# Performance work log

Measured on AMD Instinct MI355X. Metric: run time of the kernel, lower is better.

The kernel has to match this reference:

```python
import jax, jax.numpy as jnp
import numpy as np

N_HEADS = 2
EPS = 1e-5
NEG_SLOPE = 0.02
N_CENTROIDS = 1024
RADII = (0.1, 0.2)
KS = (32, 64)


def fps(x, m):
    # Farthest point sampling (deterministic start at index 0). x: [B, C, N]
    B, C, N = x.shape
    def body(carry, _):
        distance, farthest = carry
        centroid = jnp.take_along_axis(x, jnp.broadcast_to(farthest[:, None, None], (B, C, 1)), axis=2)
        dist = jnp.sum((x - centroid) ** 2, axis=1)  # [B, N]
        distance = jnp.minimum(distance, dist)
        nxt = jnp.argmax(distance, axis=1).astype(jnp.int32)
        return (distance, nxt), farthest
    init = (jnp.full((B, N), 1e10, x.dtype), jnp.zeros((B,), jnp.int32))
    _, idxs = jax.lax.scan(body, init, None, length=m)
    return idxs.T  # [B, m]


def ball_group(x, centroids, radius, k):
    # x: [B, C, N], centroids: [B, C, M] -> (idx [B,M,k] int32, mask [B,M,k] bool)
    B, C, N = x.shape
    M = centroids.shape[2]
    d = (jnp.sum(x * x, axis=1)[:, None, :]
         - 2.0 * jnp.einsum('bcm,bcn->bmn', centroids, x)
         + jnp.sum(centroids * centroids, axis=1)[:, :, None])  # [B, M, N]
    idx = jnp.broadcast_to(jnp.arange(N, dtype=jnp.int32)[None, None, :], (B, M, N))
    idx = jnp.where(d > radius * radius, N, idx)
    idx = -jax.lax.top_k(-idx, k)[0]  # k smallest indices, ascending (matches torch.topk largest=False)
    mask = idx == N
    first = jnp.where(idx[:, :, :1] == N, 0, idx[:, :, :1])
    idx = jnp.where(mask, jnp.broadcast_to(first, idx.shape), idx)
    return idx, mask


def attention_mix(x, y, mask, wq, wk, wv, wo):
    # x: [B, C, K] centroids, y: [B, C, K, Np] groups, mask: [B, K, Np]
    B, C, K = x.shape
    Np = y.shape[3]
    H = N_HEADS
    q = jnp.einsum('oc,bck->bok', wq, x).reshape(B, H, C, K)
    kk = jnp.einsum('oc,bckn->bokn', wk, y).reshape(B, H, C, K, Np)
    v = jnp.einsum('oc,bckn->bokn', wv, y).reshape(B, H, C, K, Np)
    w = jnp.einsum('bhck,bhckn->bhkn', q, kk) / (C ** 0.5)
    w = jnp.where(mask[:, None, :, :], -1e9, w)
    w = jax.nn.softmax(w, axis=3)
    o = jnp.einsum('bhkn,bhckn->bhck', w, v).reshape(B, H * C, K)
    return jnp.einsum('oc,bck->bok', wo, o) + x


def conv_bn(x, w, b, g, beta, act):
    # 1x1 Conv1d + BatchNorm1d (training-mode batch stats) + optional LeakyReLU(0.02)
    x = jnp.einsum('oc,bck->bok', w, x) + b[None, :, None]
    mu = jnp.mean(x, axis=(0, 2), keepdims=True)
    var = jnp.var(x, axis=(0, 2), keepdims=True)
    x = (x - mu) * jax.lax.rsqrt(var + EPS) * g[None, :, None] + beta[None, :, None]
    return jnp.where(x > 0, x, NEG_SLOPE * x) if act else x


def pointnet_msg(xyz, point_features, attn_params, mlp_params):
    support = jnp.concatenate([xyz, point_features], axis=1)  # [B, 32, N]
    B, Cs, N = support.shape
    M = N_CENTROIDS
    cidx = fps(support, M)  # [B, M]
    centroids = jnp.take_along_axis(support, jnp.broadcast_to(cidx[:, None, :], (B, Cs, M)), axis=2)
    new_xyz = jnp.take_along_axis(xyz, jnp.broadcast_to(cidx[:, None, :], (B, 3, M)), axis=2)
    feats = []
    for s, (radius, k) in enumerate(zip(RADII, KS)):
        idx, mask = ball_group(support, centroids, radius, k)  # [B, M, k]
        gidx = jnp.broadcast_to(idx.reshape(B, 1, M * k), (B, Cs, M * k))
        group = jnp.take_along_axis(support, gidx, axis=2).reshape(B, Cs, M, k)
        group = group - centroids[:, :, :, None]
        f = attention_mix(centroids, group, mask, *attn_params[s])
        (w0, b0, g0, t0), (w1, b1, g1, t1) = mlp_params[s]
        f = conv_bn(f, w0, b0, g0, t0, act=True)
        f = conv_bn(f, w1, b1, g1, t1, act=False)
        feats.append(f)
    return new_xyz, jnp.concatenate(feats, axis=1)  # [B,3,M], [B,256,M]


def setup_inputs() -> dict:
    key = jax.random.key(0)
    ks = jax.random.split(key, 32)
    B, N, C = 4, 16384, 32
    d = {}
    d['xyz'] = jax.random.uniform(ks[0], (B, 3, N), jnp.float32)
    d['point_features'] = jax.random.normal(ks[1], (B, C - 3, N), jnp.float32)
    i = 2
    for s in range(2):
        d[f'aq{s}'] = 0.05 * jax.random.normal(ks[i], (64, 32), jnp.float32); i += 1
        d[f'ak{s}'] = 0.05 * jax.random.normal(ks[i], (64, 32), jnp.float32); i += 1
        d[f'av{s}'] = 0.05 * jax.random.normal(ks[i], (64, 32), jnp.float32); i += 1
        d[f'ao{s}'] = 0.05 * jax.random.normal(ks[i], (32, 64), jnp.float32); i += 1
        d[f'mw{s}0'] = 0.05 * jax.random.normal(ks[i], (64, 32), jnp.float32); i += 1
        d[f'mb{s}0'] = jnp.zeros((64,), jnp.float32)
        d[f'mg{s}0'] = jnp.ones((64,), jnp.float32)
        d[f'mbt{s}0'] = jnp.zeros((64,), jnp.float32)
        d[f'mw{s}1'] = 0.05 * jax.random.normal(ks[i], (128, 64), jnp.float32); i += 1
        d[f'mb{s}1'] = jnp.zeros((128,), jnp.float32)
        d[f'mg{s}1'] = jnp.ones((128,), jnp.float32)
        d[f'mbt{s}1'] = jnp.zeros((128,), jnp.float32)
    return d


def reference(xyz, point_features,
              aq0, ak0, av0, ao0, mw00, mb00, mg00, mbt00, mw01, mb01, mg01, mbt01,
              aq1, ak1, av1, ao1, mw10, mb10, mg10, mbt10, mw11, mb11, mg11, mbt11):
    attn_params = (((aq0, ak0, av0, ao0)), ((aq1, ak1, av1, ao1)))
    mlp_params = (((mw00, mb00, mg00, mbt00), (mw01, mb01, mg01, mbt01)),
                  ((mw10, mb10, mg10, mbt10), (mw11, mb11, mg11, mbt11)))
    return pointnet_msg(xyz, point_features, attn_params, mlp_params)
```

## Files before the change

### kernel.cpp

```cpp
#include <hip/hip_runtime.h>
#include <hip/hip_bf16.h>


static constexpr int Bb = 4;
static constexpr int Npts = 16384;
static constexpr int Mc = 1024;
static constexpr int NBLK = 16;
static constexpr int OUT_EXPECT = 12288 + 1048576;
#define BN_EPS 1e-5f
#define SLOPE 0.02f
#define SCOPE_AGT __HIP_MEMORY_SCOPE_AGENT

static constexpr size_t OFF_STATS = 33024;
static constexpr size_t OFF_NORM  = 36864;
static constexpr size_t ZERO_BYTES = 65536;
static constexpr size_t OFF_CIDX  = 65536;
static constexpr size_t OFF_IDX0  = 81920;
static constexpr size_t OFF_CNT0  = 344064;
static constexpr size_t OFF_IDX1  = 360448;
static constexpr size_t OFF_CNT1  = 884736;
static constexpr size_t OFF_ATTN  = 901120;
static constexpr size_t OFF_Z0    = 1163264;
static constexpr size_t WS_REQUIRED = 1687552;
static constexpr size_t OFF_FSLOT = 901120;
static constexpr size_t FSLOT_BYTES = (size_t)Bb * Mc * NBLK * 8;

__device__ __forceinline__ float sup_at(const float* xyz, const float* pf,
                                        int b, int c, int n) {
  return (c < 3) ? xyz[((size_t)b*3 + c)*Npts + n]
                 : pf[((size_t)b*29 + (c-3))*Npts + n];
}

__device__ __forceinline__ float sanf(float v, float repl) {
  if (!(v == v) || fabsf(v) > 1e30f) v = repl;
  return v;
}

__global__ __launch_bounds__(256) void fill_kernel(float* out, int n, float val) {
  int i = blockIdx.x * 256 + threadIdx.x;
  if (i < n) out[i] = val;
}

__global__ __launch_bounds__(512, 2) void fps_kernel(
    const float* __restrict__ xyz, const float* __restrict__ pf,
    int* __restrict__ cidx, unsigned long long* __restrict__ slots) {
  const int blk = blockIdx.x;
  const int b = blk >> 4;
  const int sb = blk & (NBLK - 1);
  const int tid = threadIdx.x;
  const int lane = tid & 63, wid = tid >> 6;
  float f0[32], f1[32];
  const int p0 = sb * 1024 + tid;
  const int p1 = p0 + 512;
  float d0 = 1e10f, d1 = 1e10f;
#pragma unroll
  for (int c = 0; c < 32; ++c) {
    f0[c] = sup_at(xyz, pf, b, c, p0);
    f1[c] = sup_at(xyz, pf, b, c, p1);
  }
  __shared__ float cf[32];
  __shared__ unsigned long long red[8];
  if (sb == 0 && tid == 0) cidx[b * Mc] = 0;
  if (tid < 32) cf[tid] = sup_at(xyz, pf, b, tid, 0);
  __syncthreads();
  unsigned long long* slotb = slots + (size_t)b * Mc * NBLK;
  for (int it = 0; it < Mc - 1; ++it) {
    float cc[32];
#pragma unroll
    for (int c = 0; c < 32; ++c) cc[c] = cf[c];
    {
      float d = 0.f, e = 0.f;
#pragma unroll
      for (int c = 0; c < 32; ++c) {
        float t0 = f0[c] - cc[c];
        float s0 = __fmul_rn(t0, t0);
        d = (c == 0) ? s0 : __fadd_rn(d, s0);
        float t1 = f1[c] - cc[c];
        float s1 = __fmul_rn(t1, t1);
        e = (c == 0) ? s1 : __fadd_rn(e, s1);
      }
      d0 = fminf(d0, d);
      d1 = fminf(d1, e);
    }
    float bd; int bp;
    if (d0 >= d1) { bd = d0; bp = p0; } else { bd = d1; bp = p1; }
    unsigned long long v =
        ((unsigned long long)__float_as_uint(bd) << 32) | (unsigned int)(~(unsigned int)bp);
#pragma unroll
    for (int d = 32; d; d >>= 1) {
      unsigned long long o = __shfl_xor(v, d, 64);
      if (o > v) v = o;
    }
    if (lane == 0) red[wid] = v;
    __syncthreads();
    if (tid == 0) {
      unsigned long long vb = red[0];
#pragma unroll
      for (int w = 1; w < 8; ++w) if (red[w] > vb) vb = red[w];
      atomicMax(&slotb[(size_t)it * NBLK + sb], vb);
    }
    if (wid == 0) {
      unsigned long long myv = 0;
      if (lane < NBLK) {
        const unsigned long long* sp = &slotb[(size_t)it * NBLK + lane];
        while ((myv = __hip_atomic_load(sp, __ATOMIC_RELAXED, SCOPE_AGT)) == 0ull)
          __builtin_amdgcn_s_sleep(1);
      }
      unsigned long long mv = myv;
#pragma unroll
      for (int d = 8; d; d >>= 1) {
        unsigned long long o = __shfl_xor(mv, d, 16);
        if (o > mv) mv = o;
      }
      unsigned long long vwin = __shfl(mv, 0, 64);
      int idxWin = (int)(~(unsigned int)(vwin & 0xffffffffu)) & (Npts - 1);
      if (lane < 32) cf[lane] = sup_at(xyz, pf, b, lane, idxWin);
      if (lane == 0 && sb == 0) cidx[b * Mc + it + 1] = idxWin;
    }
    __syncthreads();
  }
}

__global__ __launch_bounds__(256) void gather_kernel(
    const float* __restrict__ xyz, const int* __restrict__ cidx,
    float* __restrict__ oxyz, int out_size) {
  int idx = blockIdx.x * 256 + threadIdx.x;
  if (idx >= out_size || idx >= 12288) return;
  int m = idx & (Mc - 1);
  int t = idx >> 10;
  int b = t / 3;
  int ci = cidx[b * Mc + m] & (Npts - 1);
  oxyz[idx] = sanf(xyz[(size_t)t * Npts + ci], 888.0f);
}

__global__ __launch_bounds__(256) void ball_kernel(
    const float* __restrict__ xyz, const float* __restrict__ pf,
    const int* __restrict__ cidx,
    unsigned short* __restrict__ idx0, int* __restrict__ cnt0,
    unsigned short* __restrict__ idx1, int* __restrict__ cnt1) {
  const int b = blockIdx.x >> 6;
  const int mt = blockIdx.x & 63;
  const int tid = threadIdx.x;
  __shared__ float cf[16][32];
  __shared__ float csq[16];
  __shared__ unsigned int ent[16][128];
  __shared__ int lcnt[16];
  for (int i = tid; i < 16 * 32; i += 256) {
    int ml = i >> 5, c = i & 31;
    int ci = cidx[b * Mc + mt * 16 + ml] & (Npts - 1);
    cf[ml][c] = sup_at(xyz, pf, b, c, ci);
  }
  if (tid < 16) lcnt[tid] = 0;
  __syncthreads();
  if (tid < 16) {
    float a = 0.f;
#pragma unroll
    for (int c = 0; c < 32; ++c) a = fmaf(cf[tid][c], cf[tid][c], a);
    csq[tid] = a;
  }
  __syncthreads();
  for (int ch = 0; ch < Npts / 256; ++ch) {
    int p = ch * 256 + tid;
    float x[32];
#pragma unroll
    for (int c = 0; c < 32; ++c) x[c] = sup_at(xyz, pf, b, c, p);
    float sp = 0.f;
#pragma unroll
    for (int c = 0; c < 32; ++c) sp = fmaf(x[c], x[c], sp);
#pragma unroll 4
    for (int ml = 0; ml < 16; ++ml) {
      float dot = 0.f;
#pragma unroll
      for (int c = 0; c < 32; ++c) dot = fmaf(cf[ml][c], x[c], dot);
      float d = sp - 2.0f * dot + csq[ml];
      if (d <= 0.04f) {
        int pos = atomicAdd(&lcnt[ml], 1);
        if (pos < 128) ent[ml][pos] = (unsigned int)p | (d <= 0.01f ? 0x80000000u : 0u);
      }
    }
  }
  __syncthreads();
  if (tid < 16) {
    int ml = tid;
    int nn = lcnt[ml]; if (nn > 128) nn = 128;
    for (int i = 1; i < nn; ++i) {
      unsigned int e = ent[ml][i]; unsigned int key = e & 0x7fffffffu;
      int j = i - 1;
      while (j >= 0 && (ent[ml][j] & 0x7fffffffu) > key) { ent[ml][j+1] = ent[ml][j]; --j; }
      ent[ml][j+1] = e;
    }
    int gm = b * Mc + mt * 16 + ml;
    int c1 = nn < 64 ? nn : 64;
    unsigned short first1 = nn > 0 ? (unsigned short)(ent[ml][0] & 0x7fffffffu) : 0;
    unsigned short* o1 = idx1 + (size_t)gm * 64;
    for (int j = 0; j < 64; ++j)
      o1[j] = j < c1 ? (unsigned short)(ent[ml][j] & 0x7fffffffu) : first1;
    cnt1[gm] = c1;
    unsigned short* o0 = idx0 + (size_t)gm * 32;
    int c0 = 0; unsigned short first0 = 0;
    for (int i = 0; i < nn && c0 < 32; ++i) {
      if (ent[ml][i] & 0x80000000u) {
        unsigned short nv = (unsigned short)(ent[ml][i] & 0x7fffffffu);
        if (c0 == 0) first0 = nv;
        o0[c0++] = nv;
      }
    }
    for (int j = c0; j < 32; ++j) o0[j] = first0;
    cnt0[gm] = c0;
  }
}

template <int K>
__global__ __launch_bounds__(256) void attn_kernel(
    const float* __restrict__ xyz, const float* __restrict__ pf,
    const int* __restrict__ cidx,
    const unsigned short* __restrict__ idxS, const int* __restrict__ cntS,
    const float* __restrict__ wq, const float* __restrict__ wk,
    const float* __restrict__ wv, const float* __restrict__ wo,
    __hip_bfloat16* __restrict__ outA) {
  __shared__ float WqL[64*33], WkL[64*33], WvL[64*33], WoL[32*65];
  __shared__ float xv[4][32];
  __shared__ float qv[4][64];
  __shared__ float yb[4][2][32];
  __shared__ float ov[4][64];
  __shared__ int cns[4];
  const int tid = threadIdx.x;
  const int wid = tid >> 6, lane = tid & 63;
  const int gid = blockIdx.x;
  const int b = gid >> 8;
  const int m = ((gid & 255) << 2) + wid;
  for (int i = tid; i < 2048; i += 256) {
    int r = i >> 5, c = i & 31;
    WqL[r*33 + c] = wq[i];
    WkL[r*33 + c] = wk[i];
    WvL[r*33 + c] = wv[i];
    int ro = i >> 6, co = i & 63;
    WoL[ro*65 + co] = wo[i];
  }
  if (lane < 32) {
    int ci = cidx[b * Mc + m] & (Npts - 1);
    xv[wid][lane] = sup_at(xyz, pf, b, lane, ci);
  }
  if (lane == 0) cns[wid] = cntS[b * Mc + m];
  __syncthreads();
  {
    float acc = 0.f;
#pragma unroll
    for (int c = 0; c < 32; ++c) acc = fmaf(WqL[lane*33 + c], xv[wid][c], acc);
    qv[wid][lane] = acc;
  }
  __syncthreads();
  int cnt = cns[wid];
  cnt = cnt < 1 ? 1 : (cnt > K ? K : cnt);
  const int jj = lane < K ? lane : 0;
  int nj = (int)idxS[((size_t)b*Mc + m)*K + jj] & (Npts - 1);
  float y[32];
#pragma unroll
  for (int c = 0; c < 32; ++c)
    y[c] = sup_at(xyz, pf, b, c, nj) - xv[wid][c];
  float w0 = 0.f, w1 = 0.f;
#pragma unroll 2
  for (int r = 0; r < 32; ++r) {
    float k0 = 0.f, k1 = 0.f;
#pragma unroll
    for (int c = 0; c < 32; ++c) {
      k0 = fmaf(WkL[r*33 + c], y[c], k0);
      k1 = fmaf(WkL[(r+32)*33 + c], y[c], k1);
    }
    w0 = fmaf(qv[wid][r], k0, w0);
    w1 = fmaf(qv[wid][r+32], k1, w1);
  }
  const float iscale = 0.17677669529663689f;
  w0 *= iscale; w1 *= iscale;
  if (lane >= cnt) { w0 = -1e9f; w1 = -1e9f; }
  float mx0 = w0, mx1 = w1;
#pragma unroll
  for (int d = K/2; d; d >>= 1) {
    mx0 = fmaxf(mx0, __shfl_xor(mx0, d, K));
    mx1 = fmaxf(mx1, __shfl_xor(mx1, d, K));
  }
  float e0 = __expf(w0 - mx0), e1 = __expf(w1 - mx1);
  float s0 = e0, s1 = e1;
#pragma unroll
  for (int d = K/2; d; d >>= 1) {
    s0 += __shfl_xor(s0, d, K);
    s1 += __shfl_xor(s1, d, K);
  }
  float wn0 = e0 / s0, wn1 = e1 / s1;
#pragma unroll
  for (int c = 0; c < 32; ++c) {
    float t0 = wn0 * y[c], t1 = wn1 * y[c];
#pragma unroll
    for (int d = K/2; d; d >>= 1) {
      t0 += __shfl_xor(t0, d, K);
      t1 += __shfl_xor(t1, d, K);
    }
    if (lane == 0) { yb[wid][0][c] = t0; yb[wid][1][c] = t1; }
  }
  __syncthreads();
  {
    const int h = lane >> 5;
    float a2 = 0.f;
#pragma unroll
    for (int c = 0; c < 32; ++c) a2 = fmaf(WvL[lane*33 + c], yb[wid][h][c], a2);
    ov[wid][lane] = a2;
  }
  __syncthreads();
  if (lane < 32) {
    float a3 = 0.f;
#pragma unroll
    for (int r = 0; r < 64; ++r) a3 = fmaf(WoL[lane*65 + r], ov[wid][r], a3);
    outA[((size_t)b*32 + lane)*Mc + m] = __float2bfloat16(a3 + xv[wid][lane]);
  }
}

__global__ __launch_bounds__(256) void conv0_kernel(
    const __hip_bfloat16* __restrict__ inA, const float* __restrict__ w0,
    const float* __restrict__ b0, __hip_bfloat16* __restrict__ z0,
    float* __restrict__ ssum, float* __restrict__ ssq) {
  int idx = blockIdx.x * 256 + threadIdx.x;
  int m = idx & (Mc - 1);
  int r = (idx >> 10) & 63;
  int b = idx >> 16;
  float acc = b0[r];
#pragma unroll
  for (int c = 0; c < 32; ++c)
    acc = fmaf(w0[r*32 + c], __bfloat162float(inA[((size_t)b*32 + c)*Mc + m]), acc);
  z0[((size_t)b*64 + r)*Mc + m] = __float2bfloat16(acc);
  float s = acc, q = acc * acc;
#pragma unroll
  for (int d = 32; d; d >>= 1) { s += __shfl_down(s, d, 64); q += __shfl_down(q, d, 64); }
  if ((threadIdx.x & 63) == 0) { atomicAdd(&ssum[r], s); atomicAdd(&ssq[r], q); }
}

__global__ void bnfin_kernel(const float* __restrict__ ssum, const float* __restrict__ ssq,
    const float* __restrict__ g, const float* __restrict__ beta,
    float* __restrict__ A, float* __restrict__ Bn, int nch, float invn) {
  int r = threadIdx.x;
  if (r < nch) {
    float mu = ssum[r] * invn;
    float var = ssq[r] * invn - mu * mu;
    if (var < 0.f) var = 0.f;
    float a = g[r] * rsqrtf(var + BN_EPS);
    A[r] = a;
    Bn[r] = beta[r] - mu * a;
  }
}

template <bool WRITE>
__global__ __launch_bounds__(256) void conv1_kernel(
    const __hip_bfloat16* __restrict__ z0, const float* __restrict__ A0, const float* __restrict__ B0n,
    const float* __restrict__ w1, const float* __restrict__ b1,
    float* __restrict__ ssum, float* __restrict__ ssq,
    const float* __restrict__ A1, const float* __restrict__ B1n,
    float* __restrict__ outAll, int chOff, int out_size) {
  int idx = blockIdx.x * 256 + threadIdx.x;
  int m = idx & (Mc - 1);
  int r2 = (idx >> 10) & 127;
  int b = idx >> 17;
  float acc = b1[r2];
#pragma unroll 8
  for (int r = 0; r < 64; ++r) {
    float u = fmaf(__bfloat162float(z0[((size_t)b*64 + r)*Mc + m]), A0[r], B0n[r]);
    u = u > 0.f ? u : SLOPE * u;
    acc = fmaf(w1[r2*64 + r], u, acc);
  }
  if (WRITE) {
    float v = fmaf(acc, A1[r2], B1n[r2]);
    size_t oidx = 12288 + ((size_t)b*256 + chOff + r2)*Mc + m;
    if (oidx < (size_t)out_size) outAll[oidx] = sanf(v, 777.0f);
  } else {
    float s = acc, q = acc * acc;
#pragma unroll
    for (int d = 32; d; d >>= 1) { s += __shfl_down(s, d, 64); q += __shfl_down(q, d, 64); }
    if ((threadIdx.x & 63) == 0) { atomicAdd(&ssum[r2], s); atomicAdd(&ssq[r2], q); }
  }
}

extern "C" void kernel_launch(void* const* d_in, const int* in_sizes, int n_in,
                              void* d_out, int out_size, void* d_ws, size_t ws_size,
                              hipStream_t stream) {
  float* outb = (float*)d_out;
  int fillBlocks = (out_size + 255) / 256;
  if (n_in != 26 || in_sizes[0] != Bb*3*Npts || in_sizes[1] != Bb*29*Npts
      || in_sizes[2] != 2048) {
    fill_kernel<<<fillBlocks, 256, 0, stream>>>(outb, out_size, 7777.0f);
    return;
  }
  if (out_size != OUT_EXPECT) {
    fill_kernel<<<fillBlocks, 256, 0, stream>>>(outb, out_size, 23456.0f);
    return;
  }
  if (ws_size < WS_REQUIRED) {
    fill_kernel<<<fillBlocks, 256, 0, stream>>>(outb, out_size, 12345.0f);
    return;
  }
  const float* xyz = (const float*)d_in[0];
  const float* pf  = (const float*)d_in[1];
  char* ws = (char*)d_ws;
  int* cidx = (int*)(ws + OFF_CIDX);
  unsigned short* idx0 = (unsigned short*)(ws + OFF_IDX0);
  int* cnt0 = (int*)(ws + OFF_CNT0);
  unsigned short* idx1 = (unsigned short*)(ws + OFF_IDX1);
  int* cnt1 = (int*)(ws + OFF_CNT1);
  unsigned long long* fslots = (unsigned long long*)(ws + OFF_FSLOT);
  __hip_bfloat16* attn = (__hip_bfloat16*)(ws + OFF_ATTN);
  __hip_bfloat16* z0 = (__hip_bfloat16*)(ws + OFF_Z0);

  hipMemsetAsync(ws, 0, ZERO_BYTES, stream);
  hipMemsetAsync(ws + OFF_FSLOT, 0, FSLOT_BYTES, stream);
  fps_kernel<<<Bb*NBLK, 512, 0, stream>>>(xyz, pf, cidx, fslots);
  ball_kernel<<<Bb*64, 256, 0, stream>>>(xyz, pf, cidx, idx0, cnt0, idx1, cnt1);

  for (int s = 0; s < 2; ++s) {
    const float* aq = (const float*)d_in[2 + s*12 + 0];
    const float* ak = (const float*)d_in[2 + s*12 + 1];
    const float* av = (const float*)d_in[2 + s*12 + 2];
    const float* ao = (const float*)d_in[2 + s*12 + 3];
    const float* w0 = (const float*)d_in[2 + s*12 + 4];
    const float* b0 = (const float*)d_in[2 + s*12 + 5];
    const float* g0 = (const float*)d_in[2 + s*12 + 6];
    const float* t0 = (const float*)d_in[2 + s*12 + 7];
    const float* w1 = (const float*)d_in[2 + s*12 + 8];
    const float* b1 = (const float*)d_in[2 + s*12 + 9];
    const float* g1 = (const float*)d_in[2 + s*12 + 10];
    const float* t1 = (const float*)d_in[2 + s*12 + 11];
    float* st = (float*)(ws + OFF_STATS) + (size_t)s*384;
    float* nrm = (float*)(ws + OFF_NORM) + (size_t)s*384;
    float *sum0 = st, *sq0 = st + 64, *sum1 = st + 128, *sq1 = st + 256;
    float *A0 = nrm, *B0n = nrm + 64, *A1 = nrm + 128, *B1n = nrm + 256;
    if (s == 0)
      attn_kernel<32><<<Bb*Mc/4, 256, 0, stream>>>(xyz, pf, cidx, idx0, cnt0, aq, ak, av, ao, attn);
    else
      attn_kernel<64><<<Bb*Mc/4, 256, 0, stream>>>(xyz, pf, cidx, idx1, cnt1, aq, ak, av, ao, attn);
    conv0_kernel<<<Bb*64*Mc/256, 256, 0, stream>>>(attn, w0, b0, z0, sum0, sq0);
    bnfin_kernel<<<1, 64, 0, stream>>>(sum0, sq0, g0, t0, A0, B0n, 64, 1.0f/4096.0f);
    conv1_kernel<false><<<Bb*128*Mc/256, 256, 0, stream>>>(z0, A0, B0n, w1, b1, sum1, sq1,
                                                           nullptr, nullptr, nullptr, 0, out_size);
    bnfin_kernel<<<1, 128, 0, stream>>>(sum1, sq1, g1, t1, A1, B1n, 128, 1.0f/4096.0f);
    conv1_kernel<true><<<Bb*128*Mc/256, 256, 0, stream>>>(z0, A0, B0n, w1, b1, nullptr, nullptr,
                                                          A1, B1n, outb, s*128, out_size);
  }
  gather_kernel<<<48, 256, 0, stream>>>(xyz, cidx, outb, out_size);
}
```

Before: 2.758 ms.

## Prefetch candidate centroids in parallel in FPS and fuse BN finalize into conv1

In the FPS loop, every block's threads now each poll one of the 16 per-block slots and gather that candidate's 32 features into shared memory. The winner is then chosen from shared memory, which removes a serial dependent global load after the cross-block reduction on the critical path of each of the 1023 iterations. Separately, the BN finalize kernels are folded into the conv1 kernels. When the workspace is large enough, the pre-BN conv1 output is cached in a new z1 buffer so the write pass skips recomputation. This costs extra polling traffic, shared memory and z1 storage, and z1 is only used when the workspace exceeds the previously required size.

```diff
diff --git a/kernel.cpp b/kernel.cpp
--- a/kernel.cpp
+++ b/kernel.cpp
@@ -12,7 +12,6 @@
 #define SCOPE_AGT __HIP_MEMORY_SCOPE_AGENT
 
 static constexpr size_t OFF_STATS = 33024;
-static constexpr size_t OFF_NORM  = 36864;
 static constexpr size_t ZERO_BYTES = 65536;
 static constexpr size_t OFF_CIDX  = 65536;
 static constexpr size_t OFF_IDX0  = 81920;
@@ -24,6 +23,8 @@
 static constexpr size_t WS_REQUIRED = 1687552;
 static constexpr size_t OFF_FSLOT = 901120;
 static constexpr size_t FSLOT_BYTES = (size_t)Bb * Mc * NBLK * 8;
+static constexpr size_t OFF_Z1 = 1687552;
+static constexpr size_t WS_Z1_REQUIRED = OFF_Z1 + (size_t)Bb * 128 * Mc * 4;
 
 __device__ __forceinline__ float sup_at(const float* xyz, const float* pf,
                                         int b, int c, int n) {
@@ -59,7 +60,9 @@
     f1[c] = sup_at(xyz, pf, b, c, p1);
   }
   __shared__ float cf[32];
+  __shared__ float cand[NBLK][32];
   __shared__ unsigned long long red[8];
+  __shared__ unsigned long long cval[NBLK];
   if (sb == 0 && tid == 0) cidx[b * Mc] = 0;
   if (tid < 32) cf[tid] = sup_at(xyz, pf, b, tid, 0);
   __syncthreads();
@@ -99,24 +102,24 @@
       for (int w = 1; w < 8; ++w) if (red[w] > vb) vb = red[w];
       atomicMax(&slotb[(size_t)it * NBLK + sb], vb);
     }
-    if (wid == 0) {
-      unsigned long long myv = 0;
-      if (lane < NBLK) {
-        const unsigned long long* sp = &slotb[(size_t)it * NBLK + lane];
-        while ((myv = __hip_atomic_load(sp, __ATOMIC_RELAXED, SCOPE_AGT)) == 0ull)
-          __builtin_amdgcn_s_sleep(1);
-      }
-      unsigned long long mv = myv;
-#pragma unroll
-      for (int d = 8; d; d >>= 1) {
-        unsigned long long o = __shfl_xor(mv, d, 16);
-        if (o > mv) mv = o;
-      }
-      unsigned long long vwin = __shfl(mv, 0, 64);
-      int idxWin = (int)(~(unsigned int)(vwin & 0xffffffffu)) & (Npts - 1);
-      if (lane < 32) cf[lane] = sup_at(xyz, pf, b, lane, idxWin);
-      if (lane == 0 && sb == 0) cidx[b * Mc + it + 1] = idxWin;
-    }
+    {
+      const int myslot = (wid << 1) | (lane >> 5);
+      const unsigned long long* sp = &slotb[(size_t)it * NBLK + myslot];
+      unsigned long long myv;
+      while ((myv = __hip_atomic_load(sp, __ATOMIC_RELAXED, SCOPE_AGT)) == 0ull)
+        __builtin_amdgcn_s_sleep(1);
+      int pc = (int)(~(unsigned int)(myv & 0xffffffffu)) & (Npts - 1);
+      cand[myslot][lane & 31] = sup_at(xyz, pf, b, lane & 31, pc);
+      if ((lane & 31) == 0) cval[myslot] = myv;
+    }
+    __syncthreads();
+    unsigned long long vwin = cval[0]; int wblk = 0;
+#pragma unroll
+    for (int w = 1; w < NBLK; ++w)
+      if (cval[w] > vwin) { vwin = cval[w]; wblk = w; }
+    if (tid < 32) cf[tid] = cand[wblk][tid];
+    if (sb == 0 && tid == 0)
+      cidx[b * Mc + it + 1] = (int)(~(unsigned int)(vwin & 0xffffffffu)) & (Npts - 1);
     __syncthreads();
   }
 }
@@ -333,48 +336,89 @@
   if ((threadIdx.x & 63) == 0) { atomicAdd(&ssum[r], s); atomicAdd(&ssq[r], q); }
 }
 
-__global__ void bnfin_kernel(const float* __restrict__ ssum, const float* __restrict__ ssq,
-    const float* __restrict__ g, const float* __restrict__ beta,
-    float* __restrict__ A, float* __restrict__ Bn, int nch, float invn) {
-  int r = threadIdx.x;
-  if (r < nch) {
-    float mu = ssum[r] * invn;
-    float var = ssq[r] * invn - mu * mu;
+__global__ __launch_bounds__(256) void conv1_stats_kernel(
+    const __hip_bfloat16* __restrict__ z0,
+    const float* __restrict__ ssum0, const float* __restrict__ ssq0,
+    const float* __restrict__ g0, const float* __restrict__ t0,
+    const float* __restrict__ w1, const float* __restrict__ b1,
+    float* __restrict__ z1,
+    float* __restrict__ ssum1, float* __restrict__ ssq1) {
+  __shared__ float A0s[64], B0s[64];
+  int tid = threadIdx.x;
+  if (tid < 64) {
+    float mu = ssum0[tid] * (1.0f/4096.0f);
+    float var = ssq0[tid] * (1.0f/4096.0f) - mu * mu;
     if (var < 0.f) var = 0.f;
-    float a = g[r] * rsqrtf(var + BN_EPS);
-    A[r] = a;
-    Bn[r] = beta[r] - mu * a;
-  }
-}
-
-template <bool WRITE>
-__global__ __launch_bounds__(256) void conv1_kernel(
-    const __hip_bfloat16* __restrict__ z0, const float* __restrict__ A0, const float* __restrict__ B0n,
-    const float* __restrict__ w1, const float* __restrict__ b1,
-    float* __restrict__ ssum, float* __restrict__ ssq,
-    const float* __restrict__ A1, const float* __restrict__ B1n,
-    float* __restrict__ outAll, int chOff, int out_size) {
-  int idx = blockIdx.x * 256 + threadIdx.x;
+    float a = g0[tid] * rsqrtf(var + BN_EPS);
+    A0s[tid] = a;
+    B0s[tid] = t0[tid] - mu * a;
+  }
+  __syncthreads();
+  int idx = blockIdx.x * 256 + tid;
   int m = idx & (Mc - 1);
   int r2 = (idx >> 10) & 127;
   int b = idx >> 17;
   float acc = b1[r2];
 #pragma unroll 8
   for (int r = 0; r < 64; ++r) {
-    float u = fmaf(__bfloat162float(z0[((size_t)b*64 + r)*Mc + m]), A0[r], B0n[r]);
+    float u = fmaf(__bfloat162float(z0[((size_t)b*64 + r)*Mc + m]), A0s[r], B0s[r]);
     u = u > 0.f ? u : SLOPE * u;
     acc = fmaf(w1[r2*64 + r], u, acc);
   }
-  if (WRITE) {
-    float v = fmaf(acc, A1[r2], B1n[r2]);
-    size_t oidx = 12288 + ((size_t)b*256 + chOff + r2)*Mc + m;
-    if (oidx < (size_t)out_size) outAll[oidx] = sanf(v, 777.0f);
+  if (z1) z1[idx] = acc;
+  float s = acc, q = acc * acc;
+#pragma unroll
+  for (int d = 32; d; d >>= 1) { s += __shfl_down(s, d, 64); q += __shfl_down(q, d, 64); }
+  if ((tid & 63) == 0) { atomicAdd(&ssum1[r2], s); atomicAdd(&ssq1[r2], q); }
+}
+
+__global__ __launch_bounds__(256) void conv1_write_kernel(
+    const __hip_bfloat16* __restrict__ z0, const float* __restrict__ z1,
+    const float* __restrict__ ssum0, const float* __restrict__ ssq0,
+    const float* __restrict__ g0, const float* __restrict__ t0,
+    const float* __restrict__ w1, const float* __restrict__ b1,
+    const float* __restrict__ ssum1, const float* __restrict__ ssq1,
+    const float* __restrict__ g1, const float* __restrict__ t1,
+    float* __restrict__ outAll, int chOff, int out_size) {
+  __shared__ float A0s[64], B0s[64];
+  __shared__ float ab1[2];
+  int tid = threadIdx.x;
+  int idx = blockIdx.x * 256 + tid;
+  int m = idx & (Mc - 1);
+  int r2 = (idx >> 10) & 127;
+  int b = idx >> 17;
+  if (!z1 && tid < 64) {
+    float mu = ssum0[tid] * (1.0f/4096.0f);
+    float var = ssq0[tid] * (1.0f/4096.0f) - mu * mu;
+    if (var < 0.f) var = 0.f;
+    float a = g0[tid] * rsqrtf(var + BN_EPS);
+    A0s[tid] = a;
+    B0s[tid] = t0[tid] - mu * a;
+  }
+  if (tid == 0) {
+    float mu = ssum1[r2] * (1.0f/4096.0f);
+    float var = ssq1[r2] * (1.0f/4096.0f) - mu * mu;
+    if (var < 0.f) var = 0.f;
+    float a = g1[r2] * rsqrtf(var + BN_EPS);
+    ab1[0] = a;
+    ab1[1] = t1[r2] - mu * a;
+  }
+  __syncthreads();
+  float acc;
+  if (z1) {
+    acc = z1[idx];
   } else {
-    float s = acc, q = acc * acc;
-#pragma unroll
-    for (int d = 32; d; d >>= 1) { s += __shfl_down(s, d, 64); q += __shfl_down(q, d, 64); }
-    if ((threadIdx.x & 63) == 0) { atomicAdd(&ssum[r2], s); atomicAdd(&ssq[r2], q); }
-  }
+    acc = b1[r2];
+#pragma unroll 8
+    for (int r = 0; r < 64; ++r) {
+      float u = fmaf(__bfloat162float(z0[((size_t)b*64 + r)*Mc + m]), A0s[r], B0s[r]);
+      u = u > 0.f ? u : SLOPE * u;
+      acc = fmaf(w1[r2*64 + r], u, acc);
+    }
+  }
+  float v = fmaf(acc, ab1[0], ab1[1]);
+  size_t oidx = 12288 + ((size_t)b*256 + chOff + r2)*Mc + m;
+  if (oidx < (size_t)out_size) outAll[oidx] = sanf(v, 777.0f);
 }
 
 extern "C" void kernel_launch(void* const* d_in, const int* in_sizes, int n_in,
@@ -406,6 +450,7 @@
   unsigned long long* fslots = (unsigned long long*)(ws + OFF_FSLOT);
   __hip_bfloat16* attn = (__hip_bfloat16*)(ws + OFF_ATTN);
   __hip_bfloat16* z0 = (__hip_bfloat16*)(ws + OFF_Z0);
+  float* z1 = (ws_size >= WS_Z1_REQUIRED) ? (float*)(ws + OFF_Z1) : nullptr;
 
   hipMemsetAsync(ws, 0, ZERO_BYTES, stream);
   hipMemsetAsync(ws + OFF_FSLOT, 0, FSLOT_BYTES, stream);
@@ -426,20 +471,17 @@
     const float* g1 = (const float*)d_in[2 + s*12 + 10];
     const float* t1 = (const float*)d_in[2 + s*12 + 11];
     float* st = (float*)(ws + OFF_STATS) + (size_t)s*384;
-    float* nrm = (float*)(ws + OFF_NORM) + (size_t)s*384;
     float *sum0 = st, *sq0 = st + 64, *sum1 = st + 128, *sq1 = st + 256;
-    float *A0 = nrm, *B0n = nrm + 64, *A1 = nrm + 128, *B1n = nrm + 256;
     if (s == 0)
       attn_kernel<32><<<Bb*Mc/4, 256, 0, stream>>>(xyz, pf, cidx, idx0, cnt0, aq, ak, av, ao, attn);
     else
       attn_kernel<64><<<Bb*Mc/4, 256, 0, stream>>>(xyz, pf, cidx, idx1, cnt1, aq, ak, av, ao, attn);
     conv0_kernel<<<Bb*64*Mc/256, 256, 0, stream>>>(attn, w0, b0, z0, sum0, sq0);
-    bnfin_kernel<<<1, 64, 0, stream>>>(sum0, sq0, g0, t0, A0, B0n, 64, 1.0f/4096.0f);
-    conv1_kernel<false><<<Bb*128*Mc/256, 256, 0, stream>>>(z0, A0, B0n, w1, b1, sum1, sq1,
-                                                           nullptr, nullptr, nullptr, 0, out_size);
-    bnfin_kernel<<<1, 128, 0, stream>>>(sum1, sq1, g1, t1, A1, B1n, 128, 1.0f/4096.0f);
-    conv1_kernel<true><<<Bb*128*Mc/256, 256, 0, stream>>>(z0, A0, B0n, w1, b1, nullptr, nullptr,
-                                                          A1, B1n, outb, s*128, out_size);
+    conv1_stats_kernel<<<Bb*128*Mc/256, 256, 0, stream>>>(z0, sum0, sq0, g0, t0,
+                                                          w1, b1, z1, sum1, sq1);
+    conv1_write_kernel<<<Bb*128*Mc/256, 256, 0, stream>>>(z0, z1, sum0, sq0, g0, t0,
+                                                          w1, b1, sum1, sq1, g1, t1,
+                                                          outb, s*128, out_size);
   }
   gather_kernel<<<48, 256, 0, stream>>>(xyz, cidx, outb, out_size);
 }
```

New measurement: 3.601 ms. 1.31x slower.
